# Kernel optimization log

Hardware: AMD Instinct MI355X
Metric: run time of the kernel (lower is better)

The kernel has to match this reference:

```python
import jax, jax.numpy as jnp
import numpy as np

HID = 192
HEADS = 12
INNER = HID * 64  # inner_dim = dim * dim_head(=64) per the module: 12288
SCALE = 64 ** -0.5  # module scales by default dim_head=64 regardless of true per-head dim
MASK_VAL = -1e4  # finite stand-in for -finfo.max; entmax zeroes these exactly
EPS = 1e-5


def sinusoidal_emb(n, dim, offset):
    # FixedPositionalEmbedding: cat(sin, cos) over dim/2 inverse frequencies
    inv_freq = 1.0 / (10000.0 ** (np.arange(0, dim, 2, dtype=np.float32) / dim))
    t = np.arange(n, dtype=np.float32) + offset
    sinu = t[:, None] * inv_freq[None, :]  # (n, dim/2)
    return jnp.asarray(np.concatenate([np.sin(sinu), np.cos(sinu)], axis=-1))  # (n, dim)


def entmax15(x):
    # exact alpha=1.5 entmax (Peters & Martins 2019), sort-based, over last axis
    x = x / 2.0
    x = x - jnp.max(x, axis=-1, keepdims=True)
    z = -jnp.sort(-x, axis=-1)  # descending
    n = x.shape[-1]
    k = jnp.arange(1, n + 1, dtype=x.dtype)
    cs = jnp.cumsum(z, axis=-1)
    css = jnp.cumsum(z * z, axis=-1)
    mean = cs / k
    ss = css - cs * mean  # = k * running variance
    delta = (1.0 - ss) / k
    tau = mean - jnp.sqrt(jnp.maximum(delta, 0.0))
    support = jnp.sum((tau <= z).astype(jnp.int32), axis=-1, keepdims=True)
    tau_star = jnp.take_along_axis(tau, support - 1, axis=-1)
    return jnp.square(jnp.maximum(x - tau_star, 0.0))


def setup_inputs() -> dict:
    key = jax.random.key(0)
    ks = jax.random.split(key, 8)
    b, lc, lq = 16, 512, 64
    c = jax.random.normal(ks[0], (b, lc, HID), dtype=jnp.float32)
    q = jax.random.normal(ks[1], (b, lq, HID), dtype=jnp.float32)
    c_mask = jnp.ones((b, lc), dtype=bool)
    q_mask = jnp.ones((b, lq), dtype=bool)
    g = jnp.ones((1,), dtype=jnp.float32)  # ScaleNorm gain
    s_in = HID ** -0.5
    Wq = jax.random.normal(ks[2], (HID, INNER), dtype=jnp.float32) * s_in
    Wk = jax.random.normal(ks[3], (HID, INNER), dtype=jnp.float32) * s_in
    Wv = jax.random.normal(ks[4], (HID, INNER), dtype=jnp.float32) * s_in
    Wo = jax.random.normal(ks[5], (INNER, HID), dtype=jnp.float32) * (INNER ** -0.5)
    bo = jnp.zeros((HID,), dtype=jnp.float32)
    return {"c": c, "q": q, "c_mask": c_mask, "q_mask": q_mask,
            "g": g, "Wq": Wq, "Wk": Wk, "Wv": Wv, "Wo": Wo, "bo": bo}


def reference(c, q, c_mask, q_mask, g, Wq, Wk, Wv, Wo, bo):
    b, lc, _ = c.shape
    lq = q.shape[1]
    residual = c
    # pre-norm ScaleNorm applied to x (=c) only; context q is NOT normed
    nrm = jnp.maximum(jnp.linalg.norm(c, axis=-1, keepdims=True), EPS)
    xn = c / nrm * g
    # position-infused attention: offset = k_len - q_len
    q_input = xn + sinusoidal_emb(lc, HID, lq - lc)[None]
    k_input = q + sinusoidal_emb(lq, HID, 0)[None]
    v_input = q  # v uses raw kv_input (no positional emb)
    d_head = INNER // HEADS
    qh = jnp.einsum('bie,ef->bif', q_input, Wq).reshape(b, lc, HEADS, d_head).transpose(0, 2, 1, 3)
    kh = jnp.einsum('bje,ef->bjf', k_input, Wk).reshape(b, lq, HEADS, d_head).transpose(0, 2, 1, 3)
    vh = jnp.einsum('bje,ef->bjf', v_input, Wv).reshape(b, lq, HEADS, d_head).transpose(0, 2, 1, 3)
    dots = jnp.einsum('bhid,bhjd->bhij', qh, kh) * SCALE  # (b,h,lc,lq)
    input_mask = c_mask[:, None, :, None] & q_mask[:, None, None, :]
    dots = jnp.where(input_mask, dots, MASK_VAL)
    attn = entmax15(dots)
    out = jnp.einsum('bhij,bhjd->bhid', attn, vh)
    out = out.transpose(0, 2, 1, 3).reshape(b, lc, INNER)
    out = jnp.einsum('bif,fe->bie', out, Wo) + bo
    att = out + residual  # Residual
    return jnp.concatenate([c, att], axis=-1)  # (b, lc, 2*HID)
```

## Files before the change

kernel.cpp:

```cpp
#include <hip/hip_runtime.h>


typedef __attribute__((ext_vector_type(8))) short short8;
typedef __attribute__((ext_vector_type(4))) float f32x4;
typedef unsigned short u16;

static __device__ __forceinline__ u16 f2bf(float f){
  union { float f; unsigned int i; } v; v.f = f;
  unsigned int x = v.i;
  return (u16)((x + 0x7FFFu + ((x >> 16) & 1u)) >> 16);
}
static __device__ __forceinline__ f32x4 mfma16(short8 a, short8 b, f32x4 c){
  return __builtin_amdgcn_mfma_f32_16x16x32_bf16(a, b, c, 0, 0, 0);
}
static __device__ __forceinline__ short8 cvt8(const float* p){
  float4 x = *(const float4*)p;
  float4 y = *(const float4*)(p + 4);
  short8 r;
  r[0] = (short)f2bf(x.x); r[1] = (short)f2bf(x.y);
  r[2] = (short)f2bf(x.z); r[3] = (short)f2bf(x.w);
  r[4] = (short)f2bf(y.x); r[5] = (short)f2bf(y.y);
  r[6] = (short)f2bf(y.z); r[7] = (short)f2bf(y.w);
  return r;
}

__global__ __launch_bounds__(256) void k_transpose_wo(const float* __restrict__ Wo, u16* __restrict__ WoT){
  __shared__ __align__(16) u16 tile[64][80];
  int bid = blockIdx.x;
  int dt = bid / 3, gt = bid - (bid / 3) * 3;
  int t = threadIdx.x;
  int r0 = t >> 3, c0 = (t & 7) * 8;
  #pragma unroll
  for (int p = 0; p < 2; p++){
    int r = p * 32 + r0;
    const float* src = Wo + (size_t)(dt * 64 + r) * 192 + gt * 64 + c0;
    *reinterpret_cast<short8*>(&tile[r][c0]) = cvt8(src);
  }
  __syncthreads();
  #pragma unroll
  for (int p = 0; p < 2; p++){
    int gl = p * 32 + r0;
    unsigned int w[4];
    #pragma unroll
    for (int qq = 0; qq < 4; qq++){
      unsigned int lo = tile[c0 + 2 * qq][gl];
      unsigned int hi = tile[c0 + 2 * qq + 1][gl];
      w[qq] = lo | (hi << 16);
    }
    uint4 pk; pk.x = w[0]; pk.y = w[1]; pk.z = w[2]; pk.w = w[3];
    *reinterpret_cast<uint4*>(WoT + (size_t)(gt * 64 + gl) * 12288 + dt * 64 + c0) = pk;
  }
}

__global__ __launch_bounds__(64) void k_prep(const float* __restrict__ c, const float* __restrict__ q,
                                             const float* __restrict__ gp, u16* __restrict__ qin,
                                             u16* __restrict__ kin, float* __restrict__ out){
  const float KLOG = 0.13841367062030675f;
  int row = blockIdx.x;
  int lane = threadIdx.x;
  float g = gp[0];
  if (row < 8192){
    int i = row & 511;
    const float* src = c + (size_t)row * 192;
    float x0 = src[lane], x1 = src[lane + 64], x2 = src[lane + 128];
    float* oc = out + (size_t)row * 384;
    oc[lane] = x0; oc[lane + 64] = x1; oc[lane + 128] = x2;
    float ss = x0 * x0 + x1 * x1 + x2 * x2;
    #pragma unroll
    for (int m = 1; m < 64; m <<= 1) ss += __shfl_xor(ss, m);
    float nrm = fmaxf(sqrtf(ss), 1e-5f);
    float sc = g / nrm;
    float t = (float)i - 448.0f;
    u16* dst = qin + (size_t)row * 192;
    #pragma unroll
    for (int kds = 0; kds < 3; kds++){
      int e = lane + kds * 64;
      float base = (kds == 0 ? x0 : (kds == 1 ? x1 : x2)) * sc;
      int f = (e < 96) ? e : e - 96;
      float invf = exp2f(-KLOG * (float)f);
      float ang = t * invf;
      float pe = (e < 96) ? sinf(ang) : cosf(ang);
      dst[e] = f2bf(base + pe);
    }
  } else {
    int r = row - 8192;
    int j = r & 63;
    const float* src = q + (size_t)r * 192;
    u16* dst = kin + (size_t)r * 192;
    float t = (float)j;
    #pragma unroll
    for (int kds = 0; kds < 3; kds++){
      int e = lane + kds * 64;
      int f = (e < 96) ? e : e - 96;
      float invf = exp2f(-KLOG * (float)f);
      float ang = t * invf;
      float pe = (e < 96) ? sinf(ang) : cosf(ang);
      dst[e] = f2bf(src[e] + pe);
    }
  }
}

__global__ __launch_bounds__(256) void k_mn(const float* __restrict__ Wq, const float* __restrict__ Wk,
                                            const float* __restrict__ Wv, const u16* __restrict__ WoT,
                                            u16* __restrict__ M, u16* __restrict__ Nt){
  int wid = blockIdx.x * 4 + (threadIdx.x >> 6);
  int lane = threadIdx.x & 63;
  int lid = lane & 15, quad = lane >> 4;
  int sel = wid / 432;
  int rem = wid - sel * 432;
  int h = rem / 36;
  int tl = rem - h * 36;
  int mt = tl / 6, nt = tl - (tl / 6) * 6;
  f32x4 acc[2][2];
  #pragma unroll
  for (int a = 0; a < 2; a++)
    #pragma unroll
    for (int bb = 0; bb < 2; bb++) acc[a][bb] = (f32x4){0.f, 0.f, 0.f, 0.f};

  if (sel == 0){
    const float* a0 = Wq + (size_t)(mt * 32 + lid) * 12288 + h * 1024 + quad * 8;
    const float* a1 = a0 + (size_t)16 * 12288;
    const float* b0 = Wk + (size_t)(nt * 32 + lid) * 12288 + h * 1024 + quad * 8;
    const float* b1 = b0 + (size_t)16 * 12288;
    for (int kk = 0; kk < 32; kk++){
      short8 A0 = cvt8(a0 + kk * 32);
      short8 A1 = cvt8(a1 + kk * 32);
      short8 B0 = cvt8(b0 + kk * 32);
      short8 B1 = cvt8(b1 + kk * 32);
      acc[0][0] = mfma16(A0, B0, acc[0][0]);
      acc[0][1] = mfma16(A0, B1, acc[0][1]);
      acc[1][0] = mfma16(A1, B0, acc[1][0]);
      acc[1][1] = mfma16(A1, B1, acc[1][1]);
    }
  } else {
    const float* a0 = Wv + (size_t)(mt * 32 + lid) * 12288 + h * 1024 + quad * 8;
    const float* a1 = a0 + (size_t)16 * 12288;
    const u16* b0 = WoT + (size_t)(nt * 32 + lid) * 12288 + h * 1024 + quad * 8;
    const u16* b1 = b0 + (size_t)16 * 12288;
    for (int kk = 0; kk < 32; kk++){
      short8 A0 = cvt8(a0 + kk * 32);
      short8 A1 = cvt8(a1 + kk * 32);
      short8 B0 = *(const short8*)(b0 + kk * 32);
      short8 B1 = *(const short8*)(b1 + kk * 32);
      acc[0][0] = mfma16(A0, B0, acc[0][0]);
      acc[0][1] = mfma16(A0, B1, acc[0][1]);
      acc[1][0] = mfma16(A1, B0, acc[1][0]);
      acc[1][1] = mfma16(A1, B1, acc[1][1]);
    }
  }

  if (sel == 0){
    u16* dst = M + (size_t)h * 36864;
    #pragma unroll
    for (int a = 0; a < 2; a++)
      #pragma unroll
      for (int bb = 0; bb < 2; bb++){
        int f = nt * 32 + bb * 16 + lid;
        #pragma unroll
        for (int r = 0; r < 4; r++){
          int e = mt * 32 + a * 16 + quad * 4 + r;
          dst[(size_t)e * 192 + f] = f2bf(acc[a][bb][r]);
        }
      }
  } else {
    u16* dst = Nt + (size_t)h * 36864;
    #pragma unroll
    for (int a = 0; a < 2; a++)
      #pragma unroll
      for (int bb = 0; bb < 2; bb++){
        int g  = nt * 32 + bb * 16 + lid;
        int e0 = mt * 32 + a * 16 + quad * 4;
        uint2 pk;
        pk.x = (unsigned)f2bf(acc[a][bb][0]) | ((unsigned)f2bf(acc[a][bb][1]) << 16);
        pk.y = (unsigned)f2bf(acc[a][bb][2]) | ((unsigned)f2bf(acc[a][bb][3]) << 16);
        *reinterpret_cast<uint2*>(dst + (size_t)g * 192 + e0) = pk;
      }
  }
}

__global__ __launch_bounds__(256) void k_w2u(const u16* __restrict__ M, const u16* __restrict__ Nt,
                                             const u16* __restrict__ kin, const float* __restrict__ v,
                                             u16* __restrict__ W2t, u16* __restrict__ ut){
  int wid = blockIdx.x * 4 + (threadIdx.x >> 6);
  int lane = threadIdx.x & 63;
  int lid = lane & 15, quad = lane >> 4;
  int sel = wid / 2304;
  int rem = wid - sel * 2304;
  int bh = rem / 12;
  int tl = rem - bh * 12;
  int b = bh / 12, h = bh - (bh / 12) * 12;
  f32x4 acc[2][2];
  #pragma unroll
  for (int a = 0; a < 2; a++)
    #pragma unroll
    for (int bb = 0; bb < 2; bb++) acc[a][bb] = (f32x4){0.f, 0.f, 0.f, 0.f};
  int mt, nt;

  if (sel == 0){
    mt = tl >> 1; nt = tl & 1;
    const u16* a0 = M   + (size_t)h * 36864 + (size_t)(mt * 32 + lid) * 192 + quad * 8;
    const u16* b0 = kin + (size_t)(b * 64 + nt * 32 + lid) * 192 + quad * 8;
    const u16* a1 = a0 + 16 * 192;
    const u16* b1 = b0 + 16 * 192;
    #pragma unroll
    for (int kk = 0; kk < 6; kk++){
      short8 A0 = *(const short8*)(a0 + kk * 32);
      short8 A1 = *(const short8*)(a1 + kk * 32);
      short8 B0 = *(const short8*)(b0 + kk * 32);
      short8 B1 = *(const short8*)(b1 + kk * 32);
      acc[0][0] = mfma16(A0, B0, acc[0][0]);
      acc[0][1] = mfma16(A0, B1, acc[0][1]);
      acc[1][0] = mfma16(A1, B0, acc[1][0]);
      acc[1][1] = mfma16(A1, B1, acc[1][1]);
    }
    u16* dst = W2t + (size_t)(b * 12 + h) * 12288;
    #pragma unroll
    for (int a = 0; a < 2; a++)
      #pragma unroll
      for (int bb = 0; bb < 2; bb++){
        int j  = nt * 32 + bb * 16 + lid;
        int e0 = mt * 32 + a * 16 + quad * 4;
        uint2 pk;
        pk.x = (unsigned)f2bf(acc[a][bb][0] * 0.0625f) | ((unsigned)f2bf(acc[a][bb][1] * 0.0625f) << 16);
        pk.y = (unsigned)f2bf(acc[a][bb][2] * 0.0625f) | ((unsigned)f2bf(acc[a][bb][3] * 0.0625f) << 16);
        *reinterpret_cast<uint2*>(dst + (size_t)j * 192 + e0) = pk;
      }
  } else {
    mt = tl / 6; nt = tl - (tl / 6) * 6;
    const float* a0 = v + (size_t)(b * 64 + mt * 32 + lid) * 192 + quad * 8;
    const float* a1 = a0 + 16 * 192;
    const u16* b0 = Nt + (size_t)h * 36864 + (size_t)(nt * 32 + lid) * 192 + quad * 8;
    const u16* b1 = b0 + 16 * 192;
    #pragma unroll
    for (int kk = 0; kk < 6; kk++){
      short8 A0 = cvt8(a0 + kk * 32);
      short8 A1 = cvt8(a1 + kk * 32);
      short8 B0 = *(const short8*)(b0 + kk * 32);
      short8 B1 = *(const short8*)(b1 + kk * 32);
      acc[0][0] = mfma16(A0, B0, acc[0][0]);
      acc[0][1] = mfma16(A0, B1, acc[0][1]);
      acc[1][0] = mfma16(A1, B0, acc[1][0]);
      acc[1][1] = mfma16(A1, B1, acc[1][1]);
    }
    u16* dst = ut + (size_t)(b * 12 + h) * 12288;
    #pragma unroll
    for (int a = 0; a < 2; a++)
      #pragma unroll
      for (int bb = 0; bb < 2; bb++){
        int g  = nt * 32 + bb * 16 + lid;
        int j0 = mt * 32 + a * 16 + quad * 4;
        uint2 pk;
        pk.x = (unsigned)f2bf(acc[a][bb][0]) | ((unsigned)f2bf(acc[a][bb][1]) << 16);
        pk.y = (unsigned)f2bf(acc[a][bb][2]) | ((unsigned)f2bf(acc[a][bb][3]) << 16);
        *reinterpret_cast<uint2*>(dst + (size_t)g * 64 + j0) = pk;
      }
  }
}

__global__ __launch_bounds__(256, 2) void k_attn(const u16* __restrict__ qin, const u16* __restrict__ W2t,
                                                 const u16* __restrict__ ut, const float* __restrict__ c,
                                                 const float* __restrict__ bo, float* __restrict__ out){
  __shared__ __align__(16) u16 attb[4][16][72];
  __shared__ __align__(16) float part[4][16][193];

  int b  = blockIdx.x >> 5;
  int i0 = (blockIdx.x & 31) << 4;
  int w    = threadIdx.x >> 6;
  int lane = threadIdx.x & 63;
  int lid = lane & 15, quad = lane >> 4;

  short8 qf[6];
  {
    const u16* qrow = qin + (size_t)(b * 512 + i0 + lid) * 192 + quad * 8;
    #pragma unroll
    for (int kk = 0; kk < 6; kk++) qf[kk] = *(const short8*)(qrow + kk * 32);
  }

  f32x4 acc[12];
  #pragma unroll
  for (int gt = 0; gt < 12; gt++) acc[gt] = (f32x4){0.f, 0.f, 0.f, 0.f};

  const u16* W2b = W2t + (size_t)(b * 12) * 12288;
  const u16* utb = ut  + (size_t)(b * 12) * 12288;

  for (int hh = 0; hh < 3; hh++){
    int h = w * 3 + hh;
    f32x4 d[4];
    #pragma unroll
    for (int jt = 0; jt < 4; jt++) d[jt] = (f32x4){0.f, 0.f, 0.f, 0.f};
    #pragma unroll
    for (int jt = 0; jt < 4; jt++){
      const u16* wrow = W2b + (size_t)h * 12288 + (size_t)(jt * 16 + lid) * 192 + quad * 8;
      #pragma unroll
      for (int kk = 0; kk < 6; kk++){
        short8 Wf = *(const short8*)(wrow + kk * 32);
        d[jt] = mfma16(Wf, qf[kk], d[jt]);
      }
    }

    float m = d[0][0];
    #pragma unroll
    for (int jt = 0; jt < 4; jt++)
      #pragma unroll
      for (int r = 0; r < 4; r++) m = fmaxf(m, d[jt][r]);
    m = fmaxf(m, __shfl_xor(m, 16));
    m = fmaxf(m, __shfl_xor(m, 32));
    float tau = m - 1.0f;
    for (int it = 0; it < 12; it++){
      float s1 = 0.f, s2 = 0.f;
      #pragma unroll
      for (int jt = 0; jt < 4; jt++){
        #pragma unroll
        for (int r = 0; r < 4; r++){
          float tv = fmaxf(d[jt][r] - tau, 0.f);
          s1 += tv; s2 = fmaf(tv, tv, s2);
        }
      }
      s1 += __shfl_xor(s1, 16); s2 += __shfl_xor(s2, 16);
      s1 += __shfl_xor(s1, 32); s2 += __shfl_xor(s2, 32);
      s1 = fmaxf(s1, 1e-20f);
      tau += (s2 - 1.0f) * 0.5f / s1;
    }

    asm volatile("" ::: "memory");
    #pragma unroll
    for (int jt = 0; jt < 4; jt++){
      float p0 = fmaxf(d[jt][0] - tau, 0.f);
      float p1 = fmaxf(d[jt][1] - tau, 0.f);
      float p2 = fmaxf(d[jt][2] - tau, 0.f);
      float p3 = fmaxf(d[jt][3] - tau, 0.f);
      uint2 pk;
      pk.x = (unsigned)f2bf(p0 * p0) | ((unsigned)f2bf(p1 * p1) << 16);
      pk.y = (unsigned)f2bf(p2 * p2) | ((unsigned)f2bf(p3 * p3) << 16);
      *reinterpret_cast<uint2*>(&attb[w][lid][jt * 16 + quad * 4]) = pk;
    }
    asm volatile("s_waitcnt lgkmcnt(0)" ::: "memory");
    __builtin_amdgcn_sched_barrier(0);

    short8 A0 = *(const short8*)&attb[w][lid][quad * 8];
    short8 A1 = *(const short8*)&attb[w][lid][quad * 8 + 32];
    #pragma unroll
    for (int gt = 0; gt < 12; gt++){
      const u16* urow = utb + (size_t)h * 12288 + (size_t)(gt * 16 + lid) * 64 + quad * 8;
      short8 B0 = *(const short8*)(urow);
      short8 B1 = *(const short8*)(urow + 32);
      acc[gt] = mfma16(A0, B0, acc[gt]);
      acc[gt] = mfma16(A1, B1, acc[gt]);
    }
  }

  #pragma unroll
  for (int gt = 0; gt < 12; gt++){
    #pragma unroll
    for (int r = 0; r < 4; r++)
      part[w][quad * 4 + r][gt * 16 + lid] = acc[gt][r];
  }
  __syncthreads();
  {
    int ti = threadIdx.x >> 4;
    int e0 = (threadIdx.x & 15) * 12;
    size_t base = (size_t)(b * 512 + i0 + ti);
    #pragma unroll
    for (int k = 0; k < 12; k++){
      int e = e0 + k;
      float s = part[0][ti][e] + part[1][ti][e] + part[2][ti][e] + part[3][ti][e];
      out[base * 384 + 192 + e] = s + bo[e] + c[base * 192 + e];
    }
  }
}

extern "C" void kernel_launch(void* const* d_in, const int* in_sizes, int n_in,
                              void* d_out, int out_size, void* d_ws, size_t ws_size,
                              hipStream_t stream) {
  (void)in_sizes; (void)n_in; (void)out_size; (void)ws_size;
  const float* c  = (const float*)d_in[0];
  const float* q  = (const float*)d_in[1];
  const float* g  = (const float*)d_in[4];
  const float* Wq = (const float*)d_in[5];
  const float* Wk = (const float*)d_in[6];
  const float* Wv = (const float*)d_in[7];
  const float* Wo = (const float*)d_in[8];
  const float* bo = (const float*)d_in[9];
  float* out = (float*)d_out;

  u16* ws  = (u16*)d_ws;
  u16* WoT = ws;
  u16* ut  = ws;
  u16* M   = ws  + 2359296;
  u16* Nt  = M   + 442368;
  u16* qin = Nt  + 442368;
  u16* kin = qin + 1572864;
  u16* W2t = kin + 196608;

  k_transpose_wo<<<576, 256, 0, stream>>>(Wo, WoT);
  k_prep<<<9216, 64, 0, stream>>>(c, q, g, qin, kin, out);
  k_mn<<<216, 256, 0, stream>>>(Wq, Wk, Wv, WoT, M, Nt);
  k_w2u<<<1152, 256, 0, stream>>>(M, Nt, kin, q, W2t, ut);
  k_attn<<<512, 256, 0, stream>>>(qin, W2t, ut, c, bo, out);
}
```

Measured before the change: 192.3 us.

## Precompute positional table, widen prep blocks, interleave entmax iterations across heads

The sinusoidal positional table (576x192) is now computed once by extra blocks appended to the Wo transpose kernel and read from workspace in k_prep, instead of evaluating sin/cos for every row. k_prep now packs four rows per 256-thread block. In k_attn the three heads per wave compute all score tiles first, then run the 12 entmax Newton iterations jointly so the shuffle reductions of the three heads can overlap. This raises register pressure in k_attn, since 48 score floats stay live, and adds a workspace read for the positional table.

```diff
diff --git a/kernel.cpp b/kernel.cpp
--- a/kernel.cpp
+++ b/kernel.cpp
@@ -24,9 +24,26 @@
   return r;
 }
 
-__global__ __launch_bounds__(256) void k_transpose_wo(const float* __restrict__ Wo, u16* __restrict__ WoT){
+__global__ __launch_bounds__(256) void k_transpose_wo(const float* __restrict__ Wo, u16* __restrict__ WoT,
+                                                      float* __restrict__ pos){
+  int bid = blockIdx.x;
+  if (bid >= 576){
+    const float KLOG = 0.13841367062030675f;
+    int idx = (bid - 576) * 256 + threadIdx.x;
+    #pragma unroll
+    for (int k = 0; k < 6; k++){
+      int entry = idx + k * 18432;
+      int row = entry / 192;
+      int e = entry - row * 192;
+      float t = (row < 512) ? ((float)row - 448.0f) : (float)(row - 512);
+      int f = (e < 96) ? e : e - 96;
+      float invf = exp2f(-KLOG * (float)f);
+      float ang = t * invf;
+      pos[entry] = (e < 96) ? sinf(ang) : cosf(ang);
+    }
+    return;
+  }
   __shared__ __align__(16) u16 tile[64][80];
-  int bid = blockIdx.x;
   int dt = bid / 3, gt = bid - (bid / 3) * 3;
   int t = threadIdx.x;
   int r0 = t >> 3, c0 = (t & 7) * 8;
@@ -52,16 +69,18 @@
   }
 }
 
-__global__ __launch_bounds__(64) void k_prep(const float* __restrict__ c, const float* __restrict__ q,
-                                             const float* __restrict__ gp, u16* __restrict__ qin,
-                                             u16* __restrict__ kin, float* __restrict__ out){
-  const float KLOG = 0.13841367062030675f;
-  int row = blockIdx.x;
-  int lane = threadIdx.x;
+__global__ __launch_bounds__(256) void k_prep(const float* __restrict__ c, const float* __restrict__ q,
+                                              const float* __restrict__ gp, const float* __restrict__ pos,
+                                              u16* __restrict__ qin, u16* __restrict__ kin,
+                                              float* __restrict__ out){
+  int w = threadIdx.x >> 6;
+  int lane = threadIdx.x & 63;
+  int row = blockIdx.x * 4 + w;
   float g = gp[0];
   if (row < 8192){
     int i = row & 511;
     const float* src = c + (size_t)row * 192;
+    const float* pr = pos + (size_t)i * 192;
     float x0 = src[lane], x1 = src[lane + 64], x2 = src[lane + 128];
     float* oc = out + (size_t)row * 384;
     oc[lane] = x0; oc[lane + 64] = x1; oc[lane + 128] = x2;
@@ -70,32 +89,20 @@
     for (int m = 1; m < 64; m <<= 1) ss += __shfl_xor(ss, m);
     float nrm = fmaxf(sqrtf(ss), 1e-5f);
     float sc = g / nrm;
-    float t = (float)i - 448.0f;
     u16* dst = qin + (size_t)row * 192;
-    #pragma unroll
-    for (int kds = 0; kds < 3; kds++){
-      int e = lane + kds * 64;
-      float base = (kds == 0 ? x0 : (kds == 1 ? x1 : x2)) * sc;
-      int f = (e < 96) ? e : e - 96;
-      float invf = exp2f(-KLOG * (float)f);
-      float ang = t * invf;
-      float pe = (e < 96) ? sinf(ang) : cosf(ang);
-      dst[e] = f2bf(base + pe);
-    }
+    dst[lane]       = f2bf(x0 * sc + pr[lane]);
+    dst[lane + 64]  = f2bf(x1 * sc + pr[lane + 64]);
+    dst[lane + 128] = f2bf(x2 * sc + pr[lane + 128]);
   } else {
     int r = row - 8192;
     int j = r & 63;
     const float* src = q + (size_t)r * 192;
+    const float* pr = pos + (size_t)(512 + j) * 192;
     u16* dst = kin + (size_t)r * 192;
-    float t = (float)j;
     #pragma unroll
     for (int kds = 0; kds < 3; kds++){
       int e = lane + kds * 64;
-      int f = (e < 96) ? e : e - 96;
-      float invf = exp2f(-KLOG * (float)f);
-      float ang = t * invf;
-      float pe = (e < 96) ? sinf(ang) : cosf(ang);
-      dst[e] = f2bf(src[e] + pe);
+      dst[e] = f2bf(src[e] + pr[e]);
     }
   }
 }
@@ -283,52 +290,71 @@
   const u16* W2b = W2t + (size_t)(b * 12) * 12288;
   const u16* utb = ut  + (size_t)(b * 12) * 12288;
 
+  f32x4 d[3][4];
+  #pragma unroll
   for (int hh = 0; hh < 3; hh++){
     int h = w * 3 + hh;
-    f32x4 d[4];
-    #pragma unroll
-    for (int jt = 0; jt < 4; jt++) d[jt] = (f32x4){0.f, 0.f, 0.f, 0.f};
     #pragma unroll
     for (int jt = 0; jt < 4; jt++){
+      f32x4 t = (f32x4){0.f, 0.f, 0.f, 0.f};
       const u16* wrow = W2b + (size_t)h * 12288 + (size_t)(jt * 16 + lid) * 192 + quad * 8;
       #pragma unroll
       for (int kk = 0; kk < 6; kk++){
         short8 Wf = *(const short8*)(wrow + kk * 32);
-        d[jt] = mfma16(Wf, qf[kk], d[jt]);
-      }
-    }
-
-    float m = d[0][0];
+        t = mfma16(Wf, qf[kk], t);
+      }
+      d[hh][jt] = t;
+    }
+  }
+
+  float tau[3];
+  #pragma unroll
+  for (int hh = 0; hh < 3; hh++){
+    float m = d[hh][0][0];
     #pragma unroll
     for (int jt = 0; jt < 4; jt++)
       #pragma unroll
-      for (int r = 0; r < 4; r++) m = fmaxf(m, d[jt][r]);
+      for (int r = 0; r < 4; r++) m = fmaxf(m, d[hh][jt][r]);
     m = fmaxf(m, __shfl_xor(m, 16));
     m = fmaxf(m, __shfl_xor(m, 32));
-    float tau = m - 1.0f;
-    for (int it = 0; it < 12; it++){
-      float s1 = 0.f, s2 = 0.f;
+    tau[hh] = m - 1.0f;
+  }
+  for (int it = 0; it < 12; it++){
+    float s1[3], s2[3];
+    #pragma unroll
+    for (int hh = 0; hh < 3; hh++){
+      float a = 0.f, bq = 0.f;
       #pragma unroll
       for (int jt = 0; jt < 4; jt++){
         #pragma unroll
         for (int r = 0; r < 4; r++){
-          float tv = fmaxf(d[jt][r] - tau, 0.f);
-          s1 += tv; s2 = fmaf(tv, tv, s2);
+          float tv = fmaxf(d[hh][jt][r] - tau[hh], 0.f);
+          a += tv; bq = fmaf(tv, tv, bq);
         }
       }
-      s1 += __shfl_xor(s1, 16); s2 += __shfl_xor(s2, 16);
-      s1 += __shfl_xor(s1, 32); s2 += __shfl_xor(s2, 32);
-      s1 = fmaxf(s1, 1e-20f);
-      tau += (s2 - 1.0f) * 0.5f / s1;
-    }
-
+      s1[hh] = a; s2[hh] = bq;
+    }
+    #pragma unroll
+    for (int hh = 0; hh < 3; hh++){ s1[hh] += __shfl_xor(s1[hh], 16); s2[hh] += __shfl_xor(s2[hh], 16); }
+    #pragma unroll
+    for (int hh = 0; hh < 3; hh++){ s1[hh] += __shfl_xor(s1[hh], 32); s2[hh] += __shfl_xor(s2[hh], 32); }
+    #pragma unroll
+    for (int hh = 0; hh < 3; hh++){
+      float s = fmaxf(s1[hh], 1e-20f);
+      tau[hh] += (s2[hh] - 1.0f) * 0.5f / s;
+    }
+  }
+
+  #pragma unroll
+  for (int hh = 0; hh < 3; hh++){
+    int h = w * 3 + hh;
     asm volatile("" ::: "memory");
     #pragma unroll
     for (int jt = 0; jt < 4; jt++){
-      float p0 = fmaxf(d[jt][0] - tau, 0.f);
-      float p1 = fmaxf(d[jt][1] - tau, 0.f);
-      float p2 = fmaxf(d[jt][2] - tau, 0.f);
-      float p3 = fmaxf(d[jt][3] - tau, 0.f);
+      float p0 = fmaxf(d[hh][jt][0] - tau[hh], 0.f);
+      float p1 = fmaxf(d[hh][jt][1] - tau[hh], 0.f);
+      float p2 = fmaxf(d[hh][jt][2] - tau[hh], 0.f);
+      float p3 = fmaxf(d[hh][jt][3] - tau[hh], 0.f);
       uint2 pk;
       pk.x = (unsigned)f2bf(p0 * p0) | ((unsigned)f2bf(p1 * p1) << 16);
       pk.y = (unsigned)f2bf(p2 * p2) | ((unsigned)f2bf(p3 * p3) << 16);
@@ -391,9 +417,10 @@
   u16* qin = Nt  + 442368;
   u16* kin = qin + 1572864;
   u16* W2t = kin + 196608;
-
-  k_transpose_wo<<<576, 256, 0, stream>>>(Wo, WoT);
-  k_prep<<<9216, 64, 0, stream>>>(c, q, g, qin, kin, out);
+  float* pos = (float*)(W2t + 2359296);
+
+  k_transpose_wo<<<648, 256, 0, stream>>>(Wo, WoT, pos);
+  k_prep<<<2304, 256, 0, stream>>>(c, q, g, pos, qin, kin, out);
   k_mn<<<216, 256, 0, stream>>>(Wq, Wk, Wv, WoT, M, Nt);
   k_w2u<<<1152, 256, 0, stream>>>(M, Nt, kin, q, W2t, ut);
   k_attn<<<512, 256, 0, stream>>>(qin, W2t, ut, c, bo, out);
```

After: 194.7 us. About the same (+1.3%).

## Pre-convert weights to bf16 in a merged prep kernel and retile the weight-product GEMM

Applied to the files above, without the earlier changes.

Merges the Wo transpose and the activation prep into one kernel that also converts Wq, Wk, Wv and q to bf16 in the workspace. The weight-product GEMM then reads bf16 directly, and each block now covers one head and one 32-row tile, with four warps each computing 48 columns. This removes one launch and the repeated fp32 loads and conversions inside the GEMM loop. In exchange it adds an extra write and read pass of roughly 14M bf16 elements through memory, and the GEMM grid shrinks from 216 to 144 blocks.

```diff
diff --git a/kernel.cpp b/kernel.cpp
--- a/kernel.cpp
+++ b/kernel.cpp
@@ -24,40 +24,60 @@
   return r;
 }
 
-__global__ __launch_bounds__(256) void k_transpose_wo(const float* __restrict__ Wo, u16* __restrict__ WoT){
+__global__ __launch_bounds__(256) void k_prep_all(
+    const float* __restrict__ Wq, const float* __restrict__ Wk, const float* __restrict__ Wv,
+    const float* __restrict__ Wo, const float* __restrict__ q, const float* __restrict__ c,
+    const float* __restrict__ gp,
+    u16* __restrict__ wqb, u16* __restrict__ wkb, u16* __restrict__ wvb,
+    u16* __restrict__ WoT, u16* __restrict__ qb,
+    u16* __restrict__ qin, u16* __restrict__ kin, float* __restrict__ out){
   __shared__ __align__(16) u16 tile[64][80];
   int bid = blockIdx.x;
-  int dt = bid / 3, gt = bid - (bid / 3) * 3;
-  int t = threadIdx.x;
-  int r0 = t >> 3, c0 = (t & 7) * 8;
-  #pragma unroll
-  for (int p = 0; p < 2; p++){
-    int r = p * 32 + r0;
-    const float* src = Wo + (size_t)(dt * 64 + r) * 192 + gt * 64 + c0;
-    *reinterpret_cast<short8*>(&tile[r][c0]) = cvt8(src);
-  }
-  __syncthreads();
-  #pragma unroll
-  for (int p = 0; p < 2; p++){
-    int gl = p * 32 + r0;
-    unsigned int w[4];
-    #pragma unroll
-    for (int qq = 0; qq < 4; qq++){
-      unsigned int lo = tile[c0 + 2 * qq][gl];
-      unsigned int hi = tile[c0 + 2 * qq + 1][gl];
-      w[qq] = lo | (hi << 16);
-    }
-    uint4 pk; pk.x = w[0]; pk.y = w[1]; pk.z = w[2]; pk.w = w[3];
-    *reinterpret_cast<uint4*>(WoT + (size_t)(gt * 64 + gl) * 12288 + dt * 64 + c0) = pk;
-  }
-}
-
-__global__ __launch_bounds__(64) void k_prep(const float* __restrict__ c, const float* __restrict__ q,
-                                             const float* __restrict__ gp, u16* __restrict__ qin,
-                                             u16* __restrict__ kin, float* __restrict__ out){
+
+  if (bid < 3552){
+    size_t t = (size_t)bid * 256 + threadIdx.x;
+    size_t base = t * 8;
+    const float* src; u16* dst; size_t off;
+    if (base < 2359296){ src = Wq; dst = wqb; off = base; }
+    else if (base < 4718592){ src = Wk; dst = wkb; off = base - 2359296; }
+    else if (base < 7077888){ src = Wv; dst = wvb; off = base - 4718592; }
+    else { src = q; dst = qb; off = base - 7077888; }
+    *reinterpret_cast<short8*>(dst + off) = cvt8(src + off);
+    return;
+  }
+
+  if (bid < 4128){
+    int tb = bid - 3552;
+    int dt = tb / 3, gt = tb - (tb / 3) * 3;
+    int t = threadIdx.x;
+    int r0 = t >> 3, c0 = (t & 7) * 8;
+    #pragma unroll
+    for (int p = 0; p < 2; p++){
+      int r = p * 32 + r0;
+      const float* src = Wo + (size_t)(dt * 64 + r) * 192 + gt * 64 + c0;
+      *reinterpret_cast<short8*>(&tile[r][c0]) = cvt8(src);
+    }
+    __syncthreads();
+    #pragma unroll
+    for (int p = 0; p < 2; p++){
+      int gl = p * 32 + r0;
+      unsigned int wv4[4];
+      #pragma unroll
+      for (int qq = 0; qq < 4; qq++){
+        unsigned int lo = tile[c0 + 2 * qq][gl];
+        unsigned int hi = tile[c0 + 2 * qq + 1][gl];
+        wv4[qq] = lo | (hi << 16);
+      }
+      uint4 pk; pk.x = wv4[0]; pk.y = wv4[1]; pk.z = wv4[2]; pk.w = wv4[3];
+      *reinterpret_cast<uint4*>(WoT + (size_t)(gt * 64 + gl) * 12288 + dt * 64 + c0) = pk;
+    }
+    return;
+  }
+
   const float KLOG = 0.13841367062030675f;
-  int row = blockIdx.x;
-  int lane = threadIdx.x;
+  int w = threadIdx.x >> 6;
+  int lane = threadIdx.x & 63;
+  int row = (bid - 4128) * 4 + w;
   float g = gp[0];
   if (row < 8192){
     int i = row & 511;
@@ -100,53 +120,38 @@
   }
 }
 
-__global__ __launch_bounds__(256) void k_mn(const float* __restrict__ Wq, const float* __restrict__ Wk,
-                                            const float* __restrict__ Wv, const u16* __restrict__ WoT,
-                                            u16* __restrict__ M, u16* __restrict__ Nt){
-  int wid = blockIdx.x * 4 + (threadIdx.x >> 6);
+__global__ __launch_bounds__(256) void k_mn2(const u16* __restrict__ wqb, const u16* __restrict__ wkb,
+                                             const u16* __restrict__ wvb, const u16* __restrict__ WoT,
+                                             u16* __restrict__ M, u16* __restrict__ Nt){
+  int bid = blockIdx.x;
+  int sh = bid % 24;
+  int mt = bid / 24;
+  int sel = sh / 12, h = sh - 12 * (sh / 12);
+  int w = threadIdx.x >> 6;
   int lane = threadIdx.x & 63;
   int lid = lane & 15, quad = lane >> 4;
-  int sel = wid / 432;
-  int rem = wid - sel * 432;
-  int h = rem / 36;
-  int tl = rem - h * 36;
-  int mt = tl / 6, nt = tl - (tl / 6) * 6;
-  f32x4 acc[2][2];
+
+  const u16* A = (sel ? wvb : wqb) + (size_t)(mt * 32 + lid) * 12288 + h * 1024 + quad * 8;
+  const u16* B = (sel ? WoT : wkb) + (size_t)(w * 48 + lid) * 12288 + h * 1024 + quad * 8;
+
+  f32x4 acc[2][3];
   #pragma unroll
   for (int a = 0; a < 2; a++)
     #pragma unroll
-    for (int bb = 0; bb < 2; bb++) acc[a][bb] = (f32x4){0.f, 0.f, 0.f, 0.f};
-
-  if (sel == 0){
-    const float* a0 = Wq + (size_t)(mt * 32 + lid) * 12288 + h * 1024 + quad * 8;
-    const float* a1 = a0 + (size_t)16 * 12288;
-    const float* b0 = Wk + (size_t)(nt * 32 + lid) * 12288 + h * 1024 + quad * 8;
-    const float* b1 = b0 + (size_t)16 * 12288;
-    for (int kk = 0; kk < 32; kk++){
-      short8 A0 = cvt8(a0 + kk * 32);
-      short8 A1 = cvt8(a1 + kk * 32);
-      short8 B0 = cvt8(b0 + kk * 32);
-      short8 B1 = cvt8(b1 + kk * 32);
-      acc[0][0] = mfma16(A0, B0, acc[0][0]);
-      acc[0][1] = mfma16(A0, B1, acc[0][1]);
-      acc[1][0] = mfma16(A1, B0, acc[1][0]);
-      acc[1][1] = mfma16(A1, B1, acc[1][1]);
-    }
-  } else {
-    const float* a0 = Wv + (size_t)(mt * 32 + lid) * 12288 + h * 1024 + quad * 8;
-    const float* a1 = a0 + (size_t)16 * 12288;
-    const u16* b0 = WoT + (size_t)(nt * 32 + lid) * 12288 + h * 1024 + quad * 8;
-    const u16* b1 = b0 + (size_t)16 * 12288;
-    for (int kk = 0; kk < 32; kk++){
-      short8 A0 = cvt8(a0 + kk * 32);
-      short8 A1 = cvt8(a1 + kk * 32);
-      short8 B0 = *(const short8*)(b0 + kk * 32);
-      short8 B1 = *(const short8*)(b1 + kk * 32);
-      acc[0][0] = mfma16(A0, B0, acc[0][0]);
-      acc[0][1] = mfma16(A0, B1, acc[0][1]);
-      acc[1][0] = mfma16(A1, B0, acc[1][0]);
-      acc[1][1] = mfma16(A1, B1, acc[1][1]);
-    }
+    for (int ct = 0; ct < 3; ct++) acc[a][ct] = (f32x4){0.f, 0.f, 0.f, 0.f};
+
+  for (int kk = 0; kk < 32; kk++){
+    short8 A0 = *(const short8*)(A + kk * 32);
+    short8 A1 = *(const short8*)(A + (size_t)16 * 12288 + kk * 32);
+    short8 B0 = *(const short8*)(B + kk * 32);
+    short8 B1 = *(const short8*)(B + (size_t)16 * 12288 + kk * 32);
+    short8 B2 = *(const short8*)(B + (size_t)32 * 12288 + kk * 32);
+    acc[0][0] = mfma16(A0, B0, acc[0][0]);
+    acc[0][1] = mfma16(A0, B1, acc[0][1]);
+    acc[0][2] = mfma16(A0, B2, acc[0][2]);
+    acc[1][0] = mfma16(A1, B0, acc[1][0]);
+    acc[1][1] = mfma16(A1, B1, acc[1][1]);
+    acc[1][2] = mfma16(A1, B2, acc[1][2]);
   }
 
   if (sel == 0){
@@ -154,12 +159,12 @@
     #pragma unroll
     for (int a = 0; a < 2; a++)
       #pragma unroll
-      for (int bb = 0; bb < 2; bb++){
-        int f = nt * 32 + bb * 16 + lid;
+      for (int ct = 0; ct < 3; ct++){
+        int f = w * 48 + ct * 16 + lid;
         #pragma unroll
         for (int r = 0; r < 4; r++){
           int e = mt * 32 + a * 16 + quad * 4 + r;
-          dst[(size_t)e * 192 + f] = f2bf(acc[a][bb][r]);
+          dst[(size_t)e * 192 + f] = f2bf(acc[a][ct][r]);
         }
       }
   } else {
@@ -167,19 +172,19 @@
     #pragma unroll
     for (int a = 0; a < 2; a++)
       #pragma unroll
-      for (int bb = 0; bb < 2; bb++){
-        int g  = nt * 32 + bb * 16 + lid;
+      for (int ct = 0; ct < 3; ct++){
+        int g  = w * 48 + ct * 16 + lid;
         int e0 = mt * 32 + a * 16 + quad * 4;
         uint2 pk;
-        pk.x = (unsigned)f2bf(acc[a][bb][0]) | ((unsigned)f2bf(acc[a][bb][1]) << 16);
-        pk.y = (unsigned)f2bf(acc[a][bb][2]) | ((unsigned)f2bf(acc[a][bb][3]) << 16);
+        pk.x = (unsigned)f2bf(acc[a][ct][0]) | ((unsigned)f2bf(acc[a][ct][1]) << 16);
+        pk.y = (unsigned)f2bf(acc[a][ct][2]) | ((unsigned)f2bf(acc[a][ct][3]) << 16);
         *reinterpret_cast<uint2*>(dst + (size_t)g * 192 + e0) = pk;
       }
   }
 }
 
 __global__ __launch_bounds__(256) void k_w2u(const u16* __restrict__ M, const u16* __restrict__ Nt,
-                                             const u16* __restrict__ kin, const float* __restrict__ v,
+                                             const u16* __restrict__ kin, const u16* __restrict__ qb,
                                              u16* __restrict__ W2t, u16* __restrict__ ut){
   int wid = blockIdx.x * 4 + (threadIdx.x >> 6);
   int lane = threadIdx.x & 63;
@@ -227,14 +232,14 @@
       }
   } else {
     mt = tl / 6; nt = tl - (tl / 6) * 6;
-    const float* a0 = v + (size_t)(b * 64 + mt * 32 + lid) * 192 + quad * 8;
-    const float* a1 = a0 + 16 * 192;
+    const u16* a0 = qb + (size_t)(b * 64 + mt * 32 + lid) * 192 + quad * 8;
+    const u16* a1 = a0 + 16 * 192;
     const u16* b0 = Nt + (size_t)h * 36864 + (size_t)(nt * 32 + lid) * 192 + quad * 8;
     const u16* b1 = b0 + 16 * 192;
     #pragma unroll
     for (int kk = 0; kk < 6; kk++){
-      short8 A0 = cvt8(a0 + kk * 32);
-      short8 A1 = cvt8(a1 + kk * 32);
+      short8 A0 = *(const short8*)(a0 + kk * 32);
+      short8 A1 = *(const short8*)(a1 + kk * 32);
       short8 B0 = *(const short8*)(b0 + kk * 32);
       short8 B1 = *(const short8*)(b1 + kk * 32);
       acc[0][0] = mfma16(A0, B0, acc[0][0]);
@@ -386,15 +391,19 @@
   u16* ws  = (u16*)d_ws;
   u16* WoT = ws;
   u16* ut  = ws;
-  u16* M   = ws  + 2359296;
+  u16* wqb = WoT + 2359296;
+  u16* W2t = wqb;
+  u16* wkb = wqb + 2359296;
+  u16* wvb = wkb + 2359296;
+  u16* qb  = wvb + 2359296;
+  u16* M   = qb  + 196608;
   u16* Nt  = M   + 442368;
   u16* qin = Nt  + 442368;
   u16* kin = qin + 1572864;
-  u16* W2t = kin + 196608;
-
-  k_transpose_wo<<<576, 256, 0, stream>>>(Wo, WoT);
-  k_prep<<<9216, 64, 0, stream>>>(c, q, g, qin, kin, out);
-  k_mn<<<216, 256, 0, stream>>>(Wq, Wk, Wv, WoT, M, Nt);
-  k_w2u<<<1152, 256, 0, stream>>>(M, Nt, kin, q, W2t, ut);
+
+  k_prep_all<<<6432, 256, 0, stream>>>(Wq, Wk, Wv, Wo, q, c, g,
+                                       wqb, wkb, wvb, WoT, qb, qin, kin, out);
+  k_mn2<<<144, 256, 0, stream>>>(wqb, wkb, wvb, WoT, M, Nt);
+  k_w2u<<<1152, 256, 0, stream>>>(M, Nt, kin, qb, W2t, ut);
   k_attn<<<512, 256, 0, stream>>>(qin, W2t, ut, c, bo, out);
 }
```

After: 181.4 us. 5.7% less time.
